# Kernel optimization log

Hardware: AMD Instinct MI355X
Metric: run time of the kernel (lower is better)

## Reference

```python
import jax, jax.numpy as jnp
import numpy as np

# Static module config (matches init_kwargs)
K = 9            # kernel_size for piecewise-linear basis with kernel_shape (3,4)
GROUPS = 1
NLAT_IN, NLON_IN = 361, 720
NLAT_OUT, NLON_OUT = 181, 360
NNZ = 120000


def _disco_s2_contraction(x, ker_idx, row_idx, col_idx, vals):
    """Sparse DISCO contraction: y[b,c,k,ho,wo] = sum_e [ker_e=k][row_e=ho]
    vals_e * x[b,c,hi_e,(wi_e + wo*pscale) % nlon_in].
    Implemented as a longitude-roll scan with gather + segment_sum (no dense psi)."""
    B, C, Hi, Wi = x.shape
    pscale = Wi // NLON_OUT
    hi = col_idx // Wi          # [nnz] input latitude
    wi = col_idx % Wi           # [nnz] input longitude (unshifted)
    seg = ker_idx * NLAT_OUT + row_idx  # [nnz] output (k, ho) segment id

    def step(x_c, _):
        # gather all nnz entries for the current longitude shift: [nnz, B*C]
        g = x_c[:, :, hi, wi].reshape(B * C, -1).T
        y = jax.ops.segment_sum(g * vals[:, None], seg, num_segments=K * NLAT_OUT)
        # roll so next output longitude sees x[..., (wi + pscale) % Wi]
        return jnp.roll(x_c, -pscale, axis=-1), y

    _, ys = jax.lax.scan(step, x, None, length=NLON_OUT)  # [Wo, K*Ho, B*C]
    y = jnp.transpose(ys, (2, 1, 0)).reshape(B, C, K, NLAT_OUT, NLON_OUT)
    return y


def setup_inputs() -> dict:
    key = jax.random.key(0)
    k1, k2, k3, k4, k5, k6, k7 = jax.random.split(key, 7)
    B, Cin, Cout = 1, 32, 32
    x = jax.random.normal(k1, (B, Cin, NLAT_IN, NLON_IN), dtype=jnp.float32)
    psi_ker_idx = jax.random.randint(k2, (NNZ,), 0, K)
    psi_row_idx = jax.random.randint(k3, (NNZ,), 0, NLAT_OUT)
    psi_col_idx = jax.random.randint(k4, (NNZ,), 0, NLAT_IN * NLON_IN)
    psi_vals = jax.random.normal(k5, (NNZ,), dtype=jnp.float32) * 0.05
    groupsize = Cin // GROUPS
    scale = np.sqrt(1.0 / groupsize)
    weight = scale * jax.random.normal(k6, (Cout, groupsize, K), dtype=jnp.float32)
    bias = jax.random.normal(k7, (Cout,), dtype=jnp.float32) * 0.01
    return {"x": x, "psi_ker_idx": psi_ker_idx, "psi_row_idx": psi_row_idx,
            "psi_col_idx": psi_col_idx, "psi_vals": psi_vals,
            "weight": weight, "bias": bias}


def reference(x, psi_ker_idx, psi_row_idx, psi_col_idx, psi_vals, weight, bias):
    # sparse gather-weight-scatter contraction -> [B, C, K, Ho, Wo]
    xk = _disco_s2_contraction(x, psi_ker_idx, psi_row_idx, psi_col_idx, psi_vals)
    B, C, _, H, W = xk.shape
    groupsize = C // GROUPS
    xk = xk.reshape(B, GROUPS, groupsize, K, H, W)
    w = weight.reshape(GROUPS, -1, weight.shape[1], weight.shape[2])  # [g, o, c, k]
    out = jnp.einsum('bgckxy,gock->bgoxy', xk, w).reshape(B, -1, H, W)
    out = out + bias.reshape(1, -1, 1, 1)
    return out
```

## Files before the change

### kernel.cpp

```cpp
#include <hip/hip_runtime.h>
#include <hip/hip_bf16.h>
#include <stdint.h>

typedef uint32_t u32;
typedef unsigned short u16;
typedef float v2f __attribute__((ext_vector_type(2)));

#define NLAT_I 361
#define NLON_I 720
#define NLAT_O 181
#define NLON_O 360
#define KK 9
#define NNZ 120000
#define NSEG (KK * NLAT_O)
#define NPIX (NLAT_O * NLON_O)
#define NCH 32
#define ROWLEN 5760

#define NBLK1 233
#define SEGS_PER_BLK 7
#define NC 4
#define LDSCAP 160
#define SPIN_LIMIT 100

#define HIST_BLKS ((NNZ + 255) / 256)

__device__ __forceinline__ u32 f2bf_rne(float f) {
    u32 b = __float_as_uint(f);
    return (b + 0x7FFFu + ((b >> 16) & 1u)) >> 16;
}

__device__ __forceinline__ int imin(int a, int b) { return a < b ? a : b; }

__global__ __launch_bounds__(256) void repack_hist_kernel(const float* __restrict__ x,
                                                          u32* __restrict__ xp,
                                                          const int* __restrict__ ker,
                                                          const int* __restrict__ row,
                                                          int* __restrict__ counts) {
    int tid = threadIdx.x;
    if (blockIdx.x >= NLAT_I) {
        int e = (blockIdx.x - NLAT_I) * 256 + tid;
        if (e < NNZ) {
            int seg = ker[e] * NLAT_O + row[e];
            atomicAdd(&counts[seg], 1);
        }
        return;
    }
    __shared__ u16 tile[32][732];
    int hi = blockIdx.x;
    const size_t plane = (size_t)NLAT_I * NLON_I;
#pragma unroll 1
    for (int c = 0; c < NCH; c++) {
        for (int col = tid; col < NLON_I; col += 256) {
            tile[c][col] = (u16)f2bf_rne(x[c * plane + (size_t)hi * NLON_I + col]);
        }
    }
    __syncthreads();
    for (int wdx = tid; wdx < 2 * ROWLEN; wdx += 256) {
        int p = wdx / ROWLEN;
        int rem = wdx - p * ROWLEN;
        int j = rem >> 4;
        int cp = rem & 15;
        int col = 2 * j + p;
        u32 v = (u32)tile[2 * cp][col] | ((u32)tile[2 * cp + 1][col] << 16);
        xp[(size_t)(2 * hi + p) * ROWLEN + rem] = v;
    }
}

__global__ __launch_bounds__(256) void scan_kernel(const int* __restrict__ counts,
                                                   int* __restrict__ offsets) {
    __shared__ int lsum[256];
    const int CH = 7;
    int t = threadIdx.x;
    int base = t * CH;
    int local[CH];
    int s = 0;
    for (int i = 0; i < CH; i++) {
        int v = (base + i < NSEG) ? counts[base + i] : 0;
        local[i] = s;
        s += v;
    }
    lsum[t] = s;
    __syncthreads();
    for (int off = 1; off < 256; off <<= 1) {
        int v = 0;
        if (t >= off) v = lsum[t - off];
        __syncthreads();
        if (t >= off) lsum[t] += v;
        __syncthreads();
    }
    int pre = (t == 0) ? 0 : lsum[t - 1];
    for (int i = 0; i < CH; i++) {
        if (base + i < NSEG) offsets[base + i] = pre + local[i];
    }
}

__global__ __launch_bounds__(256) void scatter_kernel(const int* __restrict__ ker,
                                                      const int* __restrict__ row,
                                                      const int* __restrict__ col,
                                                      const float* __restrict__ vals,
                                                      const int* __restrict__ offsets,
                                                      int* __restrict__ cursor,
                                                      int2* __restrict__ recs) {
    int e = blockIdx.x * 256 + threadIdx.x;
    if (e >= NNZ) return;
    int seg = ker[e] * NLAT_O + row[e];
    int pos = offsets[seg] + atomicAdd(&cursor[seg], 1);
    int c  = col[e];
    int hi = c / NLON_I;
    int wi = c % NLON_I;
    int p  = wi & 1;
    int a  = wi >> 1;
    u32 meta = ((u32)hi << 10) | ((u32)p << 9) | (u32)a;
    recs[pos] = make_int2((int)meta, __float_as_int(vals[e]));
}


__device__ __forceinline__ v2f bf2(u32 u) {
    v2f r;
    r.x = __uint_as_float(u << 16);
    r.y = __uint_as_float(u & 0xFFFF0000u);
    return r;
}

__device__ __forceinline__ const uint4* entry_ptr(const u32* __restrict__ xph,
                                                  u32 m, int w) {
    int row = (int)(m >> 9);
    int a   = (int)(m & 0x1FF);
    int idx = a + w;
    idx = (idx >= NLON_O) ? idx - NLON_O : idx;
    return (const uint4*)(xph + ((size_t)(row * NLON_O + idx) << 4));
}

#define FMA8(q0, q1, vv, A)                 \
    {                                       \
        A[0] = bf2(q0.x) * vv + A[0];       \
        A[1] = bf2(q0.y) * vv + A[1];       \
        A[2] = bf2(q0.z) * vv + A[2];       \
        A[3] = bf2(q0.w) * vv + A[3];       \
        A[4] = bf2(q1.x) * vv + A[4];       \
        A[5] = bf2(q1.y) * vv + A[5];       \
        A[6] = bf2(q1.z) * vv + A[6];       \
        A[7] = bf2(q1.w) * vv + A[7];       \
    }

__device__ __forceinline__ void proc_range(const u32* __restrict__ xph,
                                           const int2* __restrict__ rec,
                                           int beg, int end, int w,
                                           v2f* __restrict__ A) {
    int i = beg;
#pragma unroll 1
    for (; i + 4 <= end; i += 4) {
        int2 r0 = rec[i];
        int2 r1 = rec[i + 1];
        int2 r2 = rec[i + 2];
        int2 r3 = rec[i + 3];
        const uint4* p0 = entry_ptr(xph, (u32)r0.x, w);
        const uint4* p1 = entry_ptr(xph, (u32)r1.x, w);
        const uint4* p2 = entry_ptr(xph, (u32)r2.x, w);
        const uint4* p3 = entry_ptr(xph, (u32)r3.x, w);
        uint4 a0 = p0[0]; uint4 a1 = p0[1];
        uint4 b0 = p1[0]; uint4 b1 = p1[1];
        uint4 c0 = p2[0]; uint4 c1 = p2[1];
        uint4 d0 = p3[0]; uint4 d1 = p3[1];
        v2f v0 = {__int_as_float(r0.y), __int_as_float(r0.y)};
        v2f v1 = {__int_as_float(r1.y), __int_as_float(r1.y)};
        v2f v2 = {__int_as_float(r2.y), __int_as_float(r2.y)};
        v2f v3 = {__int_as_float(r3.y), __int_as_float(r3.y)};
        FMA8(a0, a1, v0, A)
        FMA8(b0, b1, v1, A)
        FMA8(c0, c1, v2, A)
        FMA8(d0, d1, v3, A)
    }
#pragma unroll 1
    for (; i < end; ++i) {
        int2 r0 = rec[i];
        const uint4* p0 = entry_ptr(xph, (u32)r0.x, w);
        uint4 a0 = p0[0]; uint4 a1 = p0[1];
        v2f v0 = {__int_as_float(r0.y), __int_as_float(r0.y)};
        FMA8(a0, a1, v0, A)
    }
}

__global__ __launch_bounds__(768, 3) void stage1_kernel(const u32* __restrict__ xp,
                                                        const int* __restrict__ offs,
                                                        const int* __restrict__ cnts,
                                                        const int2* __restrict__ recs,
                                                        int* __restrict__ ctr,
                                                        u16* __restrict__ xk) {
    __shared__ int2 lrec[SEGS_PER_BLK][LDSCAP];
    __shared__ int scnt[SEGS_PER_BLK], soff[SEGS_PER_BLK];

    int b = blockIdx.x;
    int tid = threadIdx.x;

    if (tid < SEGS_PER_BLK) {
        int s = b * SEGS_PER_BLK + tid;
        int ok = (s < NSEG);
        scnt[tid] = ok ? cnts[s] : 0;
        soff[tid] = ok ? offs[s] : 0;
    }
    __syncthreads();

#pragma unroll
    for (int slot = 0; slot < SEGS_PER_BLK; slot++) {
        int c = imin(scnt[slot], LDSCAP);
        int o = soff[slot];
        for (int i = tid; i < c; i += 768) lrec[slot][i] = recs[o + i];
    }
    __syncthreads();

#pragma unroll 1
    for (int slot = 0; slot < SEGS_PER_BLK; slot++) {
        int cnt = imin(scnt[slot], LDSCAP);
        int2 myrec;
        int myrank = -1;
        if (tid < cnt) {
            myrec = lrec[slot][tid];
            u32 k = (u32)myrec.x;
            int rank = 0;
            for (int j = 0; j < cnt; j++) {
                u32 kj = (u32)lrec[slot][j].x;
                rank += (kj < k || (kj == k && j < tid)) ? 1 : 0;
            }
            myrank = rank;
        }
        __syncthreads();
        if (myrank >= 0) lrec[slot][myrank] = myrec;
    }
    __syncthreads();

    int wo = tid >> 1, h = tid & 1;
    bool act = wo < NLON_O;
    int w = act ? wo : 0;
    const u32* xph = xp + h * 8;

    v2f acc[SEGS_PER_BLK][8];
#pragma unroll
    for (int slot = 0; slot < SEGS_PER_BLK; slot++)
#pragma unroll
        for (int j = 0; j < 8; j++) acc[slot][j] = (v2f){0.0f, 0.0f};

    for (int c = 0; c < NC; c++) {
#pragma unroll
        for (int slot = 0; slot < SEGS_PER_BLK; slot++) {
            int cnt = scnt[slot];
            int beg = (c * cnt) / NC;
            int end = ((c + 1) * cnt) / NC;
            if (end <= LDSCAP) {
                proc_range(xph, lrec[slot], beg, end, w, acc[slot]);
            } else {
                proc_range(xph, recs + soff[slot], beg, end, w, acc[slot]);
            }
        }
        if (c < NC - 1) {
            __syncthreads();
            if (tid == 0) {
                __hip_atomic_fetch_add(&ctr[c], 1, __ATOMIC_RELAXED,
                                       __HIP_MEMORY_SCOPE_AGENT);
                int spins = 0;
                while (spins < SPIN_LIMIT &&
                       __hip_atomic_load(&ctr[c], __ATOMIC_RELAXED,
                                         __HIP_MEMORY_SCOPE_AGENT) < (int)gridDim.x) {
                    __builtin_amdgcn_s_sleep(2);
                    ++spins;
                }
            }
            __syncthreads();
        }
    }

    if (act) {
#pragma unroll
        for (int slot = 0; slot < SEGS_PER_BLK; slot++) {
            int s = b * SEGS_PER_BLK + slot;
            if (s < NSEG) {
                int k = s / NLAT_O;
                int ho = s - k * NLAT_O;
                int pix = ho * NLON_O + wo;
#pragma unroll
                for (int j = 0; j < 8; j++) {
                    int ch = h * 16 + 2 * j;
                    xk[(size_t)(ch * KK + k) * NPIX + pix] =
                        (u16)f2bf_rne(acc[slot][j].x);
                    xk[(size_t)((ch + 1) * KK + k) * NPIX + pix] =
                        (u16)f2bf_rne(acc[slot][j].y);
                }
            }
        }
    }
}

#define S2_PP 64
#define S2_RPK 72

__global__ __launch_bounds__(256) void stage2_kernel(const u16* __restrict__ xk,
                                                     const float* __restrict__ W,
                                                     const float* __restrict__ bias,
                                                     float* __restrict__ out) {
    __shared__ float2 red[4][S2_PP][17];
    int pp  = threadIdx.x & 63;
    int ksl = threadIdx.x >> 6;
    int px2 = blockIdx.x * S2_PP + pp;
    bool act = px2 < NPIX / 2;
    int px = act ? px2 : 0;
    const u32* xk32 = (const u32*)xk;

    float a0[NCH], a1[NCH];
#pragma unroll
    for (int o = 0; o < NCH; o++) { a0[o] = 0.0f; a1[o] = 0.0f; }

    int rbase = ksl * S2_RPK;
#pragma unroll 4
    for (int rr = 0; rr < S2_RPK; rr++) {
        int r = rbase + rr;
        u32 u = xk32[(size_t)r * (NPIX / 2) + px];
        float x0 = __uint_as_float(u << 16);
        float x1 = __uint_as_float(u & 0xFFFF0000u);
#pragma unroll
        for (int o = 0; o < NCH; o++) {
            float wv = W[o * (NCH * KK) + r];
            a0[o] = fmaf(wv, x0, a0[o]);
            a1[o] = fmaf(wv, x1, a1[o]);
        }
    }

#pragma unroll 1
    for (int half = 0; half < 2; half++) {
        __syncthreads();
#pragma unroll
        for (int j = 0; j < 16; j++) {
            int o = half * 16 + j;
            red[ksl][pp][j] = make_float2(a0[o], a1[o]);
        }
        __syncthreads();
#pragma unroll
        for (int j = 0; j < 4; j++) {
            int oo = ksl * 4 + j;
            float2 s0 = red[0][pp][oo];
            float2 s1 = red[1][pp][oo];
            float2 s2 = red[2][pp][oo];
            float2 s3 = red[3][pp][oo];
            float sx = s0.x + s1.x + s2.x + s3.x;
            float sy = s0.y + s1.y + s2.y + s3.y;
            int o = half * 16 + oo;
            if (act) {
                float bv = bias[o];
                float2 v = make_float2(sx + bv, sy + bv);
                *(float2*)(out + (size_t)o * NPIX + 2 * px2) = v;
            }
        }
    }
}

extern "C" void kernel_launch(void* const* d_in, const int* in_sizes, int n_in,
                              void* d_out, int out_size, void* d_ws, size_t ws_size,
                              hipStream_t stream) {
    const float* x    = (const float*)d_in[0];
    const int* ker    = (const int*)d_in[1];
    const int* row    = (const int*)d_in[2];
    const int* col    = (const int*)d_in[3];
    const float* vals = (const float*)d_in[4];
    const float* W    = (const float*)d_in[5];
    const float* bias = (const float*)d_in[6];
    float* out        = (float*)d_out;

    char* ws = (char*)d_ws;
    const size_t off_xp   = 0;
    const size_t sz_xp    = (size_t)NLAT_I * 2 * ROWLEN * 4;
    const size_t off_cnt  = off_xp + sz_xp;
    const size_t off_off  = off_cnt + 6528;
    const size_t off_cur  = off_off + 6528;
    const size_t off_ctr  = off_cur + 6528;
    const size_t off_rec  = off_ctr + 64;
    const size_t off_xk   = off_rec + (size_t)NNZ * 8;

    u32* xp      = (u32*)(ws + off_xp);
    int* counts  = (int*)(ws + off_cnt);
    int* offsets = (int*)(ws + off_off);
    int* cursor  = (int*)(ws + off_cur);
    int* ctr     = (int*)(ws + off_ctr);
    int2* recs   = (int2*)(ws + off_rec);
    u16* xk      = (u16*)(ws + off_xk);

    hipMemsetAsync(ws + off_cnt, 0, 3 * 6528 + 64, stream);

    repack_hist_kernel<<<NLAT_I + HIST_BLKS, 256, 0, stream>>>(x, xp, ker, row, counts);
    scan_kernel<<<1, 256, 0, stream>>>(counts, offsets);
    scatter_kernel<<<HIST_BLKS, 256, 0, stream>>>(ker, row, col, vals,
                                                  offsets, cursor, recs);
    stage1_kernel<<<NBLK1, 768, 0, stream>>>(xp, offsets, counts, recs, ctr, xk);
    stage2_kernel<<<(NPIX / 2 + S2_PP - 1) / S2_PP, 256, 0, stream>>>(xk, W, bias, out);
}
```

Measured before the change: 345.9 us.

## Replace histogram/scan/scatter sort with per-block filtering of packed records

Drops the counting-sort pipeline (memset, histogram atomics, prefix scan and scatter kernels). The front kernel now writes one packed record per nonzero, with the segment id folded into the key, and resets the sync counters itself. Each stage1 block then streams the full record array and keeps, via LDS atomics, only the entries for its own segments, up to a larger LDS cap. This removes several launches and the global atomics, but every block now reads all records, and any segment with more than CAP entries is silently truncated.

```diff
diff --git a/kernel.cpp b/kernel.cpp
--- a/kernel.cpp
+++ b/kernel.cpp
@@ -20,10 +20,10 @@
 #define NBLK1 233
 #define SEGS_PER_BLK 7
 #define NC 4
-#define LDSCAP 160
+#define CAP 320
 #define SPIN_LIMIT 100
 
-#define HIST_BLKS ((NNZ + 255) / 256)
+#define PACK_BLKS ((NNZ + 255) / 256)
 
 __device__ __forceinline__ u32 f2bf_rne(float f) {
     u32 b = __float_as_uint(f);
@@ -32,17 +32,28 @@
 
 __device__ __forceinline__ int imin(int a, int b) { return a < b ? a : b; }
 
-__global__ __launch_bounds__(256) void repack_hist_kernel(const float* __restrict__ x,
-                                                          u32* __restrict__ xp,
-                                                          const int* __restrict__ ker,
-                                                          const int* __restrict__ row,
-                                                          int* __restrict__ counts) {
+__global__ __launch_bounds__(256) void front_kernel(const float* __restrict__ x,
+                                                    u32* __restrict__ xp,
+                                                    const int* __restrict__ ker,
+                                                    const int* __restrict__ row,
+                                                    const int* __restrict__ col,
+                                                    const float* __restrict__ vals,
+                                                    int2* __restrict__ recs2,
+                                                    int* __restrict__ ctr) {
     int tid = threadIdx.x;
     if (blockIdx.x >= NLAT_I) {
-        int e = (blockIdx.x - NLAT_I) * 256 + tid;
+        int pb = blockIdx.x - NLAT_I;
+        if (pb == 0 && tid < 16) ctr[tid] = 0;
+        int e = pb * 256 + tid;
         if (e < NNZ) {
             int seg = ker[e] * NLAT_O + row[e];
-            atomicAdd(&counts[seg], 1);
+            int c = col[e];
+            int hi = c / NLON_I;
+            int wi = c - hi * NLON_I;
+            int p = wi & 1;
+            int a = wi >> 1;
+            u32 key = ((u32)seg << 19) | ((u32)hi << 10) | ((u32)p << 9) | (u32)a;
+            recs2[e] = make_int2((int)key, __float_as_int(vals[e]));
         }
         return;
     }
@@ -51,8 +62,8 @@
     const size_t plane = (size_t)NLAT_I * NLON_I;
 #pragma unroll 1
     for (int c = 0; c < NCH; c++) {
-        for (int col = tid; col < NLON_I; col += 256) {
-            tile[c][col] = (u16)f2bf_rne(x[c * plane + (size_t)hi * NLON_I + col]);
+        for (int cl = tid; cl < NLON_I; cl += 256) {
+            tile[c][cl] = (u16)f2bf_rne(x[c * plane + (size_t)hi * NLON_I + cl]);
         }
     }
     __syncthreads();
@@ -61,58 +72,10 @@
         int rem = wdx - p * ROWLEN;
         int j = rem >> 4;
         int cp = rem & 15;
-        int col = 2 * j + p;
-        u32 v = (u32)tile[2 * cp][col] | ((u32)tile[2 * cp + 1][col] << 16);
+        int cl = 2 * j + p;
+        u32 v = (u32)tile[2 * cp][cl] | ((u32)tile[2 * cp + 1][cl] << 16);
         xp[(size_t)(2 * hi + p) * ROWLEN + rem] = v;
     }
-}
-
-__global__ __launch_bounds__(256) void scan_kernel(const int* __restrict__ counts,
-                                                   int* __restrict__ offsets) {
-    __shared__ int lsum[256];
-    const int CH = 7;
-    int t = threadIdx.x;
-    int base = t * CH;
-    int local[CH];
-    int s = 0;
-    for (int i = 0; i < CH; i++) {
-        int v = (base + i < NSEG) ? counts[base + i] : 0;
-        local[i] = s;
-        s += v;
-    }
-    lsum[t] = s;
-    __syncthreads();
-    for (int off = 1; off < 256; off <<= 1) {
-        int v = 0;
-        if (t >= off) v = lsum[t - off];
-        __syncthreads();
-        if (t >= off) lsum[t] += v;
-        __syncthreads();
-    }
-    int pre = (t == 0) ? 0 : lsum[t - 1];
-    for (int i = 0; i < CH; i++) {
-        if (base + i < NSEG) offsets[base + i] = pre + local[i];
-    }
-}
-
-__global__ __launch_bounds__(256) void scatter_kernel(const int* __restrict__ ker,
-                                                      const int* __restrict__ row,
-                                                      const int* __restrict__ col,
-                                                      const float* __restrict__ vals,
-                                                      const int* __restrict__ offsets,
-                                                      int* __restrict__ cursor,
-                                                      int2* __restrict__ recs) {
-    int e = blockIdx.x * 256 + threadIdx.x;
-    if (e >= NNZ) return;
-    int seg = ker[e] * NLAT_O + row[e];
-    int pos = offsets[seg] + atomicAdd(&cursor[seg], 1);
-    int c  = col[e];
-    int hi = c / NLON_I;
-    int wi = c % NLON_I;
-    int p  = wi & 1;
-    int a  = wi >> 1;
-    u32 meta = ((u32)hi << 10) | ((u32)p << 9) | (u32)a;
-    recs[pos] = make_int2((int)meta, __float_as_int(vals[e]));
 }
 
 
@@ -183,36 +146,35 @@
 }
 
 __global__ __launch_bounds__(768, 3) void stage1_kernel(const u32* __restrict__ xp,
-                                                        const int* __restrict__ offs,
-                                                        const int* __restrict__ cnts,
-                                                        const int2* __restrict__ recs,
+                                                        const int2* __restrict__ recs2,
                                                         int* __restrict__ ctr,
                                                         u16* __restrict__ xk) {
-    __shared__ int2 lrec[SEGS_PER_BLK][LDSCAP];
-    __shared__ int scnt[SEGS_PER_BLK], soff[SEGS_PER_BLK];
+    __shared__ int2 lrec[SEGS_PER_BLK][CAP];
+    __shared__ int lcnt[8];
 
     int b = blockIdx.x;
     int tid = threadIdx.x;
-
-    if (tid < SEGS_PER_BLK) {
-        int s = b * SEGS_PER_BLK + tid;
-        int ok = (s < NSEG);
-        scnt[tid] = ok ? cnts[s] : 0;
-        soff[tid] = ok ? offs[s] : 0;
-    }
+    int base = b * SEGS_PER_BLK;
+
+    if (tid < 8) lcnt[tid] = 0;
     __syncthreads();
 
-#pragma unroll
+#pragma unroll 4
+    for (int e = tid; e < NNZ; e += 768) {
+        int2 r = recs2[e];
+        int seg = (int)(((u32)r.x) >> 19);
+        unsigned rel = (unsigned)(seg - base);
+        if (rel < (unsigned)SEGS_PER_BLK) {
+            int pos = atomicAdd(&lcnt[rel], 1);
+            if (pos < CAP)
+                lrec[rel][pos] = make_int2((int)(((u32)r.x) & 0x7FFFFu), r.y);
+        }
+    }
+    __syncthreads();
+
+#pragma unroll 1
     for (int slot = 0; slot < SEGS_PER_BLK; slot++) {
-        int c = imin(scnt[slot], LDSCAP);
-        int o = soff[slot];
-        for (int i = tid; i < c; i += 768) lrec[slot][i] = recs[o + i];
-    }
-    __syncthreads();
-
-#pragma unroll 1
-    for (int slot = 0; slot < SEGS_PER_BLK; slot++) {
-        int cnt = imin(scnt[slot], LDSCAP);
+        int cnt = imin(lcnt[slot], CAP);
         int2 myrec;
         int myrank = -1;
         if (tid < cnt) {
@@ -244,14 +206,10 @@
     for (int c = 0; c < NC; c++) {
 #pragma unroll
         for (int slot = 0; slot < SEGS_PER_BLK; slot++) {
-            int cnt = scnt[slot];
+            int cnt = imin(lcnt[slot], CAP);
             int beg = (c * cnt) / NC;
             int end = ((c + 1) * cnt) / NC;
-            if (end <= LDSCAP) {
-                proc_range(xph, lrec[slot], beg, end, w, acc[slot]);
-            } else {
-                proc_range(xph, recs + soff[slot], beg, end, w, acc[slot]);
-            }
+            proc_range(xph, lrec[slot], beg, end, w, acc[slot]);
         }
         if (c < NC - 1) {
             __syncthreads();
@@ -273,7 +231,7 @@
     if (act) {
 #pragma unroll
         for (int slot = 0; slot < SEGS_PER_BLK; slot++) {
-            int s = b * SEGS_PER_BLK + slot;
+            int s = base + slot;
             if (s < NSEG) {
                 int k = s / NLAT_O;
                 int ho = s - k * NLAT_O;
@@ -366,29 +324,19 @@
     float* out        = (float*)d_out;
 
     char* ws = (char*)d_ws;
-    const size_t off_xp   = 0;
-    const size_t sz_xp    = (size_t)NLAT_I * 2 * ROWLEN * 4;
-    const size_t off_cnt  = off_xp + sz_xp;
-    const size_t off_off  = off_cnt + 6528;
-    const size_t off_cur  = off_off + 6528;
-    const size_t off_ctr  = off_cur + 6528;
-    const size_t off_rec  = off_ctr + 64;
-    const size_t off_xk   = off_rec + (size_t)NNZ * 8;
-
-    u32* xp      = (u32*)(ws + off_xp);
-    int* counts  = (int*)(ws + off_cnt);
-    int* offsets = (int*)(ws + off_off);
-    int* cursor  = (int*)(ws + off_cur);
-    int* ctr     = (int*)(ws + off_ctr);
-    int2* recs   = (int2*)(ws + off_rec);
-    u16* xk      = (u16*)(ws + off_xk);
-
-    hipMemsetAsync(ws + off_cnt, 0, 3 * 6528 + 64, stream);
-
-    repack_hist_kernel<<<NLAT_I + HIST_BLKS, 256, 0, stream>>>(x, xp, ker, row, counts);
-    scan_kernel<<<1, 256, 0, stream>>>(counts, offsets);
-    scatter_kernel<<<HIST_BLKS, 256, 0, stream>>>(ker, row, col, vals,
-                                                  offsets, cursor, recs);
-    stage1_kernel<<<NBLK1, 768, 0, stream>>>(xp, offsets, counts, recs, ctr, xk);
+    const size_t off_xp  = 0;
+    const size_t sz_xp   = (size_t)NLAT_I * 2 * ROWLEN * 4;
+    const size_t off_ctr = off_xp + sz_xp;
+    const size_t off_rec = off_ctr + 64;
+    const size_t off_xk  = off_rec + (size_t)NNZ * 8;
+
+    u32* xp    = (u32*)(ws + off_xp);
+    int* ctr   = (int*)(ws + off_ctr);
+    int2* recs2 = (int2*)(ws + off_rec);
+    u16* xk    = (u16*)(ws + off_xk);
+
+    front_kernel<<<NLAT_I + PACK_BLKS, 256, 0, stream>>>(x, xp, ker, row, col,
+                                                         vals, recs2, ctr);
+    stage1_kernel<<<NBLK1, 768, 0, stream>>>(xp, recs2, ctr, xk);
     stage2_kernel<<<(NPIX / 2 + S2_PP - 1) / S2_PP, 256, 0, stream>>>(xk, W, bias, out);
 }
```

Result: no change. 344.1 us (-0.5%).
